# Performance work log

Hardware: AMD Instinct MI355X
Metric: run time of the kernel (lower is better)

The kernel has to match this reference:

```python
import jax, jax.numpy as jnp
import numpy as np

MARGIN = 0.5  # init kwarg margin=0.5 (float -> fix_margin branch)

N, D, NUM_CLASSES = 8192, 128, 512


def setup_inputs() -> dict:
    key = jax.random.key(0)
    k1, k2 = jax.random.split(key)
    embeds = jax.random.normal(k1, (N, D), dtype=jnp.float32)
    labels = jax.random.randint(k2, (N,), 0, NUM_CLASSES)
    return {"embeds": embeds, "labels": labels}


def reference(embeds, labels):
    n = embeds.shape[0]
    # --- batch-hard mining (detached in original: .detach().cpu().numpy()) ---
    # Euclidean pairwise distances via Gram trick (avoids [N,N,D] intermediate).
    sq = jnp.sum(embeds * embeds, axis=1)  # [N]
    d2 = sq[:, None] + sq[None, :] - 2.0 * (embeds @ embeds.T)  # [N,N]
    dist = jnp.sqrt(jnp.maximum(d2, 0.0))
    dist = jax.lax.stop_gradient(dist)

    same = labels[:, None] == labels[None, :]  # [N,N]
    eye = jnp.eye(n, dtype=bool)
    pos_mask = same & ~eye          # same label, not self
    neg_mask = ~same                # different label (diag excluded since same there)

    pos_idx = jnp.argmax(jnp.where(pos_mask, dist, -jnp.inf), axis=1)  # hardest positive
    neg_idx = jnp.argmin(jnp.where(neg_mask, dist, jnp.inf), axis=1)   # hardest negative

    # --- margin loss with metric='sqeuclidean' (gradients flow through gathers) ---
    dp = embeds - embeds[pos_idx]
    dn = embeds - embeds[neg_idx]
    ap = jnp.sum(dp * dp, axis=1)
    an = jnp.sum(dn * dn, axis=1)
    return jnp.mean(jax.nn.relu(ap - an + MARGIN))
```

## Files before the change

### kernel.cpp

```cpp
#include <hip/hip_runtime.h>
#include <stdint.h>

#define NROWS 8192
#define DIM 128
#define ROWB 256
#define NIBLK 64
#define NCHUNK 32
#define MARGIN 0.5f

typedef short short8 __attribute__((ext_vector_type(8)));
typedef float f32x4 __attribute__((ext_vector_type(4)));
typedef int   int4v __attribute__((ext_vector_type(4)));

#define GLDS16(g, l) __builtin_amdgcn_global_load_lds( \
    (const __attribute__((address_space(1))) unsigned int*)(g), \
    (__attribute__((address_space(3))) unsigned int*)(l), 16, 0, 0)

static __device__ __forceinline__ unsigned short f2bf(float f) {
    union { float f; unsigned u; } x; x.f = f;
    unsigned u = x.u;
    return (unsigned short)((u + 0x7FFFu + ((u >> 16) & 1u)) >> 16);
}

__global__ __launch_bounds__(256) void prep(const float* __restrict__ emb,
                                            unsigned short* __restrict__ e16,
                                            float* __restrict__ cbuf,
                                            unsigned* __restrict__ pos,
                                            unsigned* __restrict__ neg,
                                            float* __restrict__ out) {
    const int lane = threadIdx.x & 63;
    const int row = blockIdx.x * 4 + (threadIdx.x >> 6);
    const float2 v = reinterpret_cast<const float2*>(emb + row * DIM)[lane];
    float sq = v.x * v.x + v.y * v.y;
#pragma unroll
    for (int m = 1; m < 64; m <<= 1) sq += __shfl_xor(sq, m, 64);
    const unsigned pack = ((unsigned)f2bf(v.y) << 16) | (unsigned)f2bf(v.x);
    *reinterpret_cast<unsigned*>(e16 + row * DIM + lane * 2) = pack;
    if (lane == 0) cbuf[row] = sq + 512.0f;
    if (lane == 1) pos[row] = 0u;
    if (lane == 2) neg[row] = 0xFFFFFFFFu;
    if (blockIdx.x == 0 && threadIdx.x == 0) out[0] = 0.0f;
}

__global__ __launch_bounds__(512, 6) void mine(const unsigned short* __restrict__ e16,
                                               const float* __restrict__ cbuf,
                                               const int* __restrict__ labels,
                                               unsigned* __restrict__ pos,
                                               unsigned* __restrict__ neg) {
    __shared__ char smem[2][16384];
    const int tid  = threadIdx.x;
    const int wave = tid >> 6;
    const int lane = tid & 63;
    const int l15  = lane & 15;
    const int lhi  = lane >> 4;
    const int iblk = blockIdx.x & (NIBLK - 1);
    const int cblk = blockIdx.x / NIBLK;
    const int irow = iblk * 128 + wave * 16 + l15;
    const char* e8 = (const char*)e16;
    const int jc = cblk * 256;

    {
        const char* gs = e8 + (size_t)jc * ROWB;
        char* lb = smem[0];
#pragma unroll
        for (int q = 0; q < 2; ++q) {
            const int r = q * 32 + (tid >> 4);
            const int d = tid & 15;
            const int g = d ^ (r & 15);
            GLDS16(gs + (size_t)r * ROWB + g * 16, lb + q * 8192 + tid * 16);
        }
    }

    short8 bfrag[4];
#pragma unroll
    for (int ks = 0; ks < 4; ++ks)
        bfrag[ks] = *reinterpret_cast<const short8*>(e8 + (size_t)irow * ROWB + (ks * 4 + lhi) * 16);
    const int labi = labels[irow];

    unsigned bp = 0u, bn = 0xFFFFFFFFu;

    __syncthreads();

#pragma unroll
    for (int st = 0; st < 4; ++st) {
        if (st < 3) {
            const char* gs = e8 + (size_t)(jc + (st + 1) * 64) * ROWB;
            char* lb = smem[(st + 1) & 1];
#pragma unroll
            for (int q = 0; q < 2; ++q) {
                const int r = q * 32 + (tid >> 4);
                const int d = tid & 15;
                const int g = d ^ (r & 15);
                GLDS16(gs + (size_t)r * ROWB + g * 16, lb + q * 8192 + tid * 16);
            }
        }
        const char* buf = smem[st & 1];
#pragma unroll
        for (int jt = 0; jt < 4; ++jt) {
            const int jb = jc + st * 64 + jt * 16;
            const int4v labj = *reinterpret_cast<const int4v*>(labels + jb + lhi * 4);
            const f32x4 c4   = *reinterpret_cast<const f32x4*>(cbuf + jb + lhi * 4);
            const f32x4 cinit = c4 * -0.5f;

            short8 af[4];
#pragma unroll
            for (int ks = 0; ks < 4; ++ks)
                af[ks] = *reinterpret_cast<const short8*>(
                    buf + (jt * 16 + l15) * ROWB + (((ks * 4 + lhi) ^ l15) * 16));

            f32x4 acc = __builtin_amdgcn_mfma_f32_16x16x32_bf16(af[0], bfrag[0], cinit, 0, 0, 0);
#pragma unroll
            for (int ks = 1; ks < 4; ++ks)
                acc = __builtin_amdgcn_mfma_f32_16x16x32_bf16(af[ks], bfrag[ks], acc, 0, 0, 0);

            const int j0 = jb + lhi * 4;
#pragma unroll
            for (int r = 0; r < 4; ++r) {
                union { float f; unsigned u; } cv; cv.f = acc[r];
                const unsigned cand = (cv.u & 0xFFFFE000u) | (unsigned)(j0 + r);
                const bool eq = (labj[r] == labi);
                const unsigned psel = eq ? cand : 0u;
                const unsigned nsel = eq ? 0xFFFFFFFFu : cand;
                bp = bp > psel ? bp : psel;
                bn = bn < nsel ? bn : nsel;
            }
        }
        __syncthreads();
    }

    {
        unsigned o;
        o = (unsigned)__shfl_xor((int)bp, 16, 64); bp = bp > o ? bp : o;
        o = (unsigned)__shfl_xor((int)bp, 32, 64); bp = bp > o ? bp : o;
        o = (unsigned)__shfl_xor((int)bn, 16, 64); bn = bn < o ? bn : o;
        o = (unsigned)__shfl_xor((int)bn, 32, 64); bn = bn < o ? bn : o;
    }
    if (lane < 16) {
        const int i = iblk * 128 + wave * 16 + lane;
        atomicMax(&pos[i], bp);
        atomicMin(&neg[i], bn);
    }
}

__global__ __launch_bounds__(256) void lossk(const float* __restrict__ emb,
                                             const unsigned* __restrict__ pos,
                                             const unsigned* __restrict__ neg,
                                             float* __restrict__ bsum) {
    __shared__ float wsum[4];
    const int tid = threadIdx.x, lane = tid & 63, wave = tid >> 6;
    const int i = blockIdx.x * 4 + wave;
    const int jp = (int)(pos[i] & 8191u);
    const int jn = (int)(neg[i] & 8191u);
    const float2 a = reinterpret_cast<const float2*>(emb + (size_t)i  * DIM)[lane];
    const float2 b = reinterpret_cast<const float2*>(emb + (size_t)jp * DIM)[lane];
    const float2 c = reinterpret_cast<const float2*>(emb + (size_t)jn * DIM)[lane];
    float dx = a.x - b.x, dy = a.y - b.y;
    const float ap = dx * dx + dy * dy;
    dx = a.x - c.x; dy = a.y - c.y;
    const float an = dx * dx + dy * dy;
    float s = ap - an;
#pragma unroll
    for (int m = 1; m < 64; m <<= 1) s += __shfl_xor(s, m, 64);
    if (lane == 0) wsum[wave] = fmaxf(s + MARGIN, 0.f);
    __syncthreads();
    if (tid == 0) bsum[blockIdx.x] = wsum[0] + wsum[1] + wsum[2] + wsum[3];
}

__global__ __launch_bounds__(256) void fin(const float* __restrict__ bsum,
                                           float* __restrict__ out) {
    __shared__ float wsum[4];
    const int tid = threadIdx.x, lane = tid & 63, wave = tid >> 6;
    float s = 0.f;
#pragma unroll
    for (int k = 0; k < 8; ++k) s += bsum[tid + k * 256];
#pragma unroll
    for (int m = 1; m < 64; m <<= 1) s += __shfl_xor(s, m, 64);
    if (lane == 0) wsum[wave] = s;
    __syncthreads();
    if (tid == 0) out[0] = (wsum[0] + wsum[1] + wsum[2] + wsum[3]) * (1.0f / (float)NROWS);
}

extern "C" void kernel_launch(void* const* d_in, const int* in_sizes, int n_in,
                              void* d_out, int out_size, void* d_ws, size_t ws_size,
                              hipStream_t stream) {
    const float* emb   = (const float*)d_in[0];
    const int* labels  = (const int*)d_in[1];
    float* out = (float*)d_out;
    char* ws = (char*)d_ws;

    unsigned short* e16 = (unsigned short*)ws;
    float* cbuf         = (float*)(ws + (size_t)2097152);
    unsigned* pos       = (unsigned*)(ws + (size_t)2097152 + 32768);
    unsigned* neg       = pos + NROWS;
    float* bsum         = (float*)(neg + NROWS);

    prep<<<2048, 256, 0, stream>>>(emb, e16, cbuf, pos, neg, out);
    mine<<<NIBLK * NCHUNK, 512, 0, stream>>>(e16, cbuf, labels, pos, neg);
    lossk<<<2048, 256, 0, stream>>>(emb, pos, neg, bsum);
    fin<<<1, 256, 0, stream>>>(bsum, out);
}
```

Baseline: 94.39 us.

## Compute two 16-row i-tiles per wave to reuse LDS A-fragments across MFMAs

The mining kernel drops to 256 threads per block, and each wave now handles 32 anchor rows as two 16-row register fragments. Each LDS-loaded j-fragment therefore feeds two MFMA chains, halving LDS reads per MFMA. Label and norm loads are hoisted per stage and the swizzled LDS offsets are precomputed. The cost is more registers per thread and fewer waves per block, which may lower occupancy and latency hiding.

```diff
diff --git a/kernel.cpp b/kernel.cpp
--- a/kernel.cpp
+++ b/kernel.cpp
@@ -42,7 +42,7 @@
     if (blockIdx.x == 0 && threadIdx.x == 0) out[0] = 0.0f;
 }
 
-__global__ __launch_bounds__(512, 6) void mine(const unsigned short* __restrict__ e16,
+__global__ __launch_bounds__(256, 4) void mine(const unsigned short* __restrict__ e16,
                                                const float* __restrict__ cbuf,
                                                const int* __restrict__ labels,
                                                unsigned* __restrict__ pos,
@@ -55,29 +55,39 @@
     const int lhi  = lane >> 4;
     const int iblk = blockIdx.x & (NIBLK - 1);
     const int cblk = blockIdx.x / NIBLK;
-    const int irow = iblk * 128 + wave * 16 + l15;
+    const int ibase = iblk * 128 + wave * 32;
     const char* e8 = (const char*)e16;
     const int jc = cblk * 256;
+
+    const int srow = tid >> 4;
+    const int gsw  = ((tid & 15) ^ srow) * 16;
 
     {
         const char* gs = e8 + (size_t)jc * ROWB;
         char* lb = smem[0];
 #pragma unroll
-        for (int q = 0; q < 2; ++q) {
-            const int r = q * 32 + (tid >> 4);
-            const int d = tid & 15;
-            const int g = d ^ (r & 15);
-            GLDS16(gs + (size_t)r * ROWB + g * 16, lb + q * 8192 + tid * 16);
-        }
-    }
-
-    short8 bfrag[4];
+        for (int q = 0; q < 4; ++q)
+            GLDS16(gs + (size_t)(q * 16 + srow) * ROWB + gsw, lb + q * 4096 + tid * 16);
+    }
+
+    short8 bfrag[2][4];
+    int labi[2];
+#pragma unroll
+    for (int it = 0; it < 2; ++it) {
+        const int row = ibase + it * 16 + l15;
+#pragma unroll
+        for (int ks = 0; ks < 4; ++ks)
+            bfrag[it][ks] = *reinterpret_cast<const short8*>(e8 + (size_t)row * ROWB + (ks * 4 + lhi) * 16);
+        labi[it] = labels[row];
+    }
+
+    int dsoff[4];
 #pragma unroll
     for (int ks = 0; ks < 4; ++ks)
-        bfrag[ks] = *reinterpret_cast<const short8*>(e8 + (size_t)irow * ROWB + (ks * 4 + lhi) * 16);
-    const int labi = labels[irow];
-
-    unsigned bp = 0u, bn = 0xFFFFFFFFu;
+        dsoff[ks] = l15 * ROWB + (((ks * 4 + lhi) ^ l15) * 16);
+
+    unsigned bp[2] = {0u, 0u};
+    unsigned bn[2] = {0xFFFFFFFFu, 0xFFFFFFFFu};
 
     __syncthreads();
 
@@ -87,58 +97,66 @@
             const char* gs = e8 + (size_t)(jc + (st + 1) * 64) * ROWB;
             char* lb = smem[(st + 1) & 1];
 #pragma unroll
-            for (int q = 0; q < 2; ++q) {
-                const int r = q * 32 + (tid >> 4);
-                const int d = tid & 15;
-                const int g = d ^ (r & 15);
-                GLDS16(gs + (size_t)r * ROWB + g * 16, lb + q * 8192 + tid * 16);
-            }
+            for (int q = 0; q < 4; ++q)
+                GLDS16(gs + (size_t)(q * 16 + srow) * ROWB + gsw, lb + q * 4096 + tid * 16);
+        }
+        int4v labj_s[4];
+        f32x4 cin_s[4];
+#pragma unroll
+        for (int jt = 0; jt < 4; ++jt) {
+            const int jb = jc + st * 64 + jt * 16;
+            labj_s[jt] = *reinterpret_cast<const int4v*>(labels + jb + lhi * 4);
+            cin_s[jt]  = *reinterpret_cast<const f32x4*>(cbuf + jb + lhi * 4) * -0.5f;
         }
         const char* buf = smem[st & 1];
 #pragma unroll
         for (int jt = 0; jt < 4; ++jt) {
-            const int jb = jc + st * 64 + jt * 16;
-            const int4v labj = *reinterpret_cast<const int4v*>(labels + jb + lhi * 4);
-            const f32x4 c4   = *reinterpret_cast<const f32x4*>(cbuf + jb + lhi * 4);
-            const f32x4 cinit = c4 * -0.5f;
-
             short8 af[4];
 #pragma unroll
             for (int ks = 0; ks < 4; ++ks)
-                af[ks] = *reinterpret_cast<const short8*>(
-                    buf + (jt * 16 + l15) * ROWB + (((ks * 4 + lhi) ^ l15) * 16));
-
-            f32x4 acc = __builtin_amdgcn_mfma_f32_16x16x32_bf16(af[0], bfrag[0], cinit, 0, 0, 0);
+                af[ks] = *reinterpret_cast<const short8*>(buf + jt * 4096 + dsoff[ks]);
+
+            f32x4 acc[2];
+#pragma unroll
+            for (int it = 0; it < 2; ++it)
+                acc[it] = __builtin_amdgcn_mfma_f32_16x16x32_bf16(af[0], bfrag[it][0], cin_s[jt], 0, 0, 0);
 #pragma unroll
             for (int ks = 1; ks < 4; ++ks)
-                acc = __builtin_amdgcn_mfma_f32_16x16x32_bf16(af[ks], bfrag[ks], acc, 0, 0, 0);
-
-            const int j0 = jb + lhi * 4;
-#pragma unroll
-            for (int r = 0; r < 4; ++r) {
-                union { float f; unsigned u; } cv; cv.f = acc[r];
-                const unsigned cand = (cv.u & 0xFFFFE000u) | (unsigned)(j0 + r);
-                const bool eq = (labj[r] == labi);
-                const unsigned psel = eq ? cand : 0u;
-                const unsigned nsel = eq ? 0xFFFFFFFFu : cand;
-                bp = bp > psel ? bp : psel;
-                bn = bn < nsel ? bn : nsel;
+#pragma unroll
+                for (int it = 0; it < 2; ++it)
+                    acc[it] = __builtin_amdgcn_mfma_f32_16x16x32_bf16(af[ks], bfrag[it][ks], acc[it], 0, 0, 0);
+
+            const int j0 = jc + st * 64 + jt * 16 + lhi * 4;
+#pragma unroll
+            for (int it = 0; it < 2; ++it) {
+#pragma unroll
+                for (int r = 0; r < 4; ++r) {
+                    union { float f; unsigned u; } cv; cv.f = acc[it][r];
+                    const unsigned cand = (cv.u & 0xFFFFE000u) | (unsigned)(j0 + r);
+                    const bool eq = (labj_s[jt][r] == labi[it]);
+                    const unsigned psel = eq ? cand : 0u;
+                    const unsigned nsel = eq ? 0xFFFFFFFFu : cand;
+                    bp[it] = bp[it] > psel ? bp[it] : psel;
+                    bn[it] = bn[it] < nsel ? bn[it] : nsel;
+                }
             }
         }
         __syncthreads();
     }
 
-    {
+#pragma unroll
+    for (int it = 0; it < 2; ++it) {
         unsigned o;
-        o = (unsigned)__shfl_xor((int)bp, 16, 64); bp = bp > o ? bp : o;
-        o = (unsigned)__shfl_xor((int)bp, 32, 64); bp = bp > o ? bp : o;
-        o = (unsigned)__shfl_xor((int)bn, 16, 64); bn = bn < o ? bn : o;
-        o = (unsigned)__shfl_xor((int)bn, 32, 64); bn = bn < o ? bn : o;
-    }
-    if (lane < 16) {
-        const int i = iblk * 128 + wave * 16 + lane;
-        atomicMax(&pos[i], bp);
-        atomicMin(&neg[i], bn);
+        o = (unsigned)__shfl_xor((int)bp[it], 16, 64); bp[it] = bp[it] > o ? bp[it] : o;
+        o = (unsigned)__shfl_xor((int)bp[it], 32, 64); bp[it] = bp[it] > o ? bp[it] : o;
+        o = (unsigned)__shfl_xor((int)bn[it], 16, 64); bn[it] = bn[it] < o ? bn[it] : o;
+        o = (unsigned)__shfl_xor((int)bn[it], 32, 64); bn[it] = bn[it] < o ? bn[it] : o;
+    }
+    if (lane < 32) {
+        const int it = lane >> 4;
+        const int i = ibase + lane;
+        atomicMax(&pos[i], bp[it]);
+        atomicMin(&neg[i], bn[it]);
     }
 }
 
@@ -195,7 +213,7 @@
     float* bsum         = (float*)(neg + NROWS);
 
     prep<<<2048, 256, 0, stream>>>(emb, e16, cbuf, pos, neg, out);
-    mine<<<NIBLK * NCHUNK, 512, 0, stream>>>(e16, cbuf, labels, pos, neg);
+    mine<<<NIBLK * NCHUNK, 256, 0, stream>>>(e16, cbuf, labels, pos, neg);
     lossk<<<2048, 256, 0, stream>>>(emb, pos, neg, bsum);
     fin<<<1, 256, 0, stream>>>(bsum, out);
 }
```

New measurement: 92.45 us. -2.0%, faster.

## Store embeddings in MFMA fragment order and read A-tiles directly from global

Applied to the files above, without the earlier changes.

The prep kernel now writes the bf16 embeddings in a pre-swizzled MFMA-fragment layout, so each lane loads its 16-byte fragment with one coalesced global load. The mining kernel drops the LDS double-buffer and its barriers, and each wave now holds four 16-row i-tiles in registers to reuse every loaded j-fragment across four MFMAs. This removes LDS traffic and synchronisation and raises arithmetic reuse per load, but it relies on L2/L1 caching for the repeated j-tile reads and raises register pressure with the occupancy hint reduced to 4.

```diff
diff --git a/kernel.cpp b/kernel.cpp
--- a/kernel.cpp
+++ b/kernel.cpp
@@ -3,18 +3,11 @@
 
 #define NROWS 8192
 #define DIM 128
-#define ROWB 256
-#define NIBLK 64
-#define NCHUNK 32
 #define MARGIN 0.5f
 
 typedef short short8 __attribute__((ext_vector_type(8)));
 typedef float f32x4 __attribute__((ext_vector_type(4)));
 typedef int   int4v __attribute__((ext_vector_type(4)));
-
-#define GLDS16(g, l) __builtin_amdgcn_global_load_lds( \
-    (const __attribute__((address_space(1))) unsigned int*)(g), \
-    (__attribute__((address_space(3))) unsigned int*)(l), 16, 0, 0)
 
 static __device__ __forceinline__ unsigned short f2bf(float f) {
     union { float f; unsigned u; } x; x.f = f;
@@ -23,122 +16,111 @@
 }
 
 __global__ __launch_bounds__(256) void prep(const float* __restrict__ emb,
-                                            unsigned short* __restrict__ e16,
+                                            char* __restrict__ efrag,
                                             float* __restrict__ cbuf,
                                             unsigned* __restrict__ pos,
                                             unsigned* __restrict__ neg,
                                             float* __restrict__ out) {
-    const int lane = threadIdx.x & 63;
+    const int d = threadIdx.x & 63;
     const int row = blockIdx.x * 4 + (threadIdx.x >> 6);
-    const float2 v = reinterpret_cast<const float2*>(emb + row * DIM)[lane];
+    const float2 v = reinterpret_cast<const float2*>(emb + row * DIM)[d];
     float sq = v.x * v.x + v.y * v.y;
 #pragma unroll
     for (int m = 1; m < 64; m <<= 1) sq += __shfl_xor(sq, m, 64);
     const unsigned pack = ((unsigned)f2bf(v.y) << 16) | (unsigned)f2bf(v.x);
-    *reinterpret_cast<unsigned*>(e16 + row * DIM + lane * 2) = pack;
-    if (lane == 0) cbuf[row] = sq + 512.0f;
-    if (lane == 1) pos[row] = 0u;
-    if (lane == 2) neg[row] = 0xFFFFFFFFu;
+    char* dst = efrag + (size_t)(row >> 4) * 4096 + (d >> 4) * 1024
+              + ((((d >> 2) & 3) * 16 + (row & 15)) * 16) + (d & 3) * 4;
+    *reinterpret_cast<unsigned*>(dst) = pack;
+    if (d == 0) cbuf[row] = sq + 512.0f;
+    if (d == 1) pos[row] = 0u;
+    if (d == 2) neg[row] = 0xFFFFFFFFu;
     if (blockIdx.x == 0 && threadIdx.x == 0) out[0] = 0.0f;
 }
 
-__global__ __launch_bounds__(512, 6) void mine(const unsigned short* __restrict__ e16,
+__global__ __launch_bounds__(256, 4) void mine(const char* __restrict__ efrag,
                                                const float* __restrict__ cbuf,
                                                const int* __restrict__ labels,
                                                unsigned* __restrict__ pos,
                                                unsigned* __restrict__ neg) {
-    __shared__ char smem[2][16384];
     const int tid  = threadIdx.x;
     const int wave = tid >> 6;
     const int lane = tid & 63;
     const int l15  = lane & 15;
     const int lhi  = lane >> 4;
-    const int iblk = blockIdx.x & (NIBLK - 1);
-    const int cblk = blockIdx.x / NIBLK;
-    const int irow = iblk * 128 + wave * 16 + l15;
-    const char* e8 = (const char*)e16;
+    const int iblk = blockIdx.x & 31;
+    const int cblk = blockIdx.x >> 5;
+    const int ibase = iblk * 256 + wave * 64;
+
+    short8 bfrag[4][4];
+    int labi[4];
+#pragma unroll
+    for (int it = 0; it < 4; ++it) {
+        const char* bt = efrag + (size_t)((ibase >> 4) + it) * 4096 + lane * 16;
+#pragma unroll
+        for (int ks = 0; ks < 4; ++ks)
+            bfrag[it][ks] = *reinterpret_cast<const short8*>(bt + ks * 1024);
+        labi[it] = labels[ibase + it * 16 + l15];
+    }
+
+    unsigned bp[4] = {0u, 0u, 0u, 0u};
+    unsigned bn[4] = {0xFFFFFFFFu, 0xFFFFFFFFu, 0xFFFFFFFFu, 0xFFFFFFFFu};
+
     const int jc = cblk * 256;
+    const char* aj = efrag + (size_t)(cblk * 16) * 4096 + lane * 16;
 
-    {
-        const char* gs = e8 + (size_t)jc * ROWB;
-        char* lb = smem[0];
+#pragma unroll 2
+    for (int jt = 0; jt < 16; ++jt) {
+        const int jb = jc + jt * 16;
+        const int4v labj = *reinterpret_cast<const int4v*>(labels + jb + lhi * 4);
+        const f32x4 cinit = *reinterpret_cast<const f32x4*>(cbuf + jb + lhi * 4) * -0.5f;
+        const char* at = aj + (size_t)jt * 4096;
+
+        const short8 af0 = *reinterpret_cast<const short8*>(at);
+        const short8 af1 = *reinterpret_cast<const short8*>(at + 1024);
+        f32x4 acc[4];
 #pragma unroll
-        for (int q = 0; q < 2; ++q) {
-            const int r = q * 32 + (tid >> 4);
-            const int d = tid & 15;
-            const int g = d ^ (r & 15);
-            GLDS16(gs + (size_t)r * ROWB + g * 16, lb + q * 8192 + tid * 16);
+        for (int it = 0; it < 4; ++it)
+            acc[it] = __builtin_amdgcn_mfma_f32_16x16x32_bf16(af0, bfrag[it][0], cinit, 0, 0, 0);
+#pragma unroll
+        for (int it = 0; it < 4; ++it)
+            acc[it] = __builtin_amdgcn_mfma_f32_16x16x32_bf16(af1, bfrag[it][1], acc[it], 0, 0, 0);
+        const short8 af2 = *reinterpret_cast<const short8*>(at + 2048);
+        const short8 af3 = *reinterpret_cast<const short8*>(at + 3072);
+#pragma unroll
+        for (int it = 0; it < 4; ++it)
+            acc[it] = __builtin_amdgcn_mfma_f32_16x16x32_bf16(af2, bfrag[it][2], acc[it], 0, 0, 0);
+#pragma unroll
+        for (int it = 0; it < 4; ++it)
+            acc[it] = __builtin_amdgcn_mfma_f32_16x16x32_bf16(af3, bfrag[it][3], acc[it], 0, 0, 0);
+
+        const int jv = jb + lhi * 4;
+#pragma unroll
+        for (int it = 0; it < 4; ++it) {
+#pragma unroll
+            for (int r = 0; r < 4; ++r) {
+                union { float f; unsigned u; } cv; cv.f = acc[it][r];
+                const unsigned cand = (cv.u & 0xFFFFE000u) | (unsigned)(jv + r);
+                const bool eq = (labj[r] == labi[it]);
+                const unsigned psel = eq ? cand : 0u;
+                const unsigned nsel = eq ? 0xFFFFFFFFu : cand;
+                bp[it] = bp[it] > psel ? bp[it] : psel;
+                bn[it] = bn[it] < nsel ? bn[it] : nsel;
+            }
         }
     }
 
-    short8 bfrag[4];
 #pragma unroll
-    for (int ks = 0; ks < 4; ++ks)
-        bfrag[ks] = *reinterpret_cast<const short8*>(e8 + (size_t)irow * ROWB + (ks * 4 + lhi) * 16);
-    const int labi = labels[irow];
-
-    unsigned bp = 0u, bn = 0xFFFFFFFFu;
-
-    __syncthreads();
-
-#pragma unroll
-    for (int st = 0; st < 4; ++st) {
-        if (st < 3) {
-            const char* gs = e8 + (size_t)(jc + (st + 1) * 64) * ROWB;
-            char* lb = smem[(st + 1) & 1];
-#pragma unroll
-            for (int q = 0; q < 2; ++q) {
-                const int r = q * 32 + (tid >> 4);
-                const int d = tid & 15;
-                const int g = d ^ (r & 15);
-                GLDS16(gs + (size_t)r * ROWB + g * 16, lb + q * 8192 + tid * 16);
-            }
+    for (int it = 0; it < 4; ++it) {
+        unsigned o;
+        o = (unsigned)__shfl_xor((int)bp[it], 16, 64); bp[it] = bp[it] > o ? bp[it] : o;
+        o = (unsigned)__shfl_xor((int)bp[it], 32, 64); bp[it] = bp[it] > o ? bp[it] : o;
+        o = (unsigned)__shfl_xor((int)bn[it], 16, 64); bn[it] = bn[it] < o ? bn[it] : o;
+        o = (unsigned)__shfl_xor((int)bn[it], 32, 64); bn[it] = bn[it] < o ? bn[it] : o;
+        if (lane < 16) {
+            const int i = ibase + it * 16 + lane;
+            atomicMax(&pos[i], bp[it]);
+            atomicMin(&neg[i], bn[it]);
         }
-        const char* buf = smem[st & 1];
-#pragma unroll
-        for (int jt = 0; jt < 4; ++jt) {
-            const int jb = jc + st * 64 + jt * 16;
-            const int4v labj = *reinterpret_cast<const int4v*>(labels + jb + lhi * 4);
-            const f32x4 c4   = *reinterpret_cast<const f32x4*>(cbuf + jb + lhi * 4);
-            const f32x4 cinit = c4 * -0.5f;
-
-            short8 af[4];
-#pragma unroll
-            for (int ks = 0; ks < 4; ++ks)
-                af[ks] = *reinterpret_cast<const short8*>(
-                    buf + (jt * 16 + l15) * ROWB + (((ks * 4 + lhi) ^ l15) * 16));
-
-            f32x4 acc = __builtin_amdgcn_mfma_f32_16x16x32_bf16(af[0], bfrag[0], cinit, 0, 0, 0);
-#pragma unroll
-            for (int ks = 1; ks < 4; ++ks)
-                acc = __builtin_amdgcn_mfma_f32_16x16x32_bf16(af[ks], bfrag[ks], acc, 0, 0, 0);
-
-            const int j0 = jb + lhi * 4;
-#pragma unroll
-            for (int r = 0; r < 4; ++r) {
-                union { float f; unsigned u; } cv; cv.f = acc[r];
-                const unsigned cand = (cv.u & 0xFFFFE000u) | (unsigned)(j0 + r);
-                const bool eq = (labj[r] == labi);
-                const unsigned psel = eq ? cand : 0u;
-                const unsigned nsel = eq ? 0xFFFFFFFFu : cand;
-                bp = bp > psel ? bp : psel;
-                bn = bn < nsel ? bn : nsel;
-            }
-        }
-        __syncthreads();
-    }
-
-    {
-        unsigned o;
-        o = (unsigned)__shfl_xor((int)bp, 16, 64); bp = bp > o ? bp : o;
-        o = (unsigned)__shfl_xor((int)bp, 32, 64); bp = bp > o ? bp : o;
-        o = (unsigned)__shfl_xor((int)bn, 16, 64); bn = bn < o ? bn : o;
-        o = (unsigned)__shfl_xor((int)bn, 32, 64); bn = bn < o ? bn : o;
-    }
-    if (lane < 16) {
-        const int i = iblk * 128 + wave * 16 + lane;
-        atomicMax(&pos[i], bp);
-        atomicMin(&neg[i], bn);
     }
 }
 
@@ -188,14 +170,14 @@
     float* out = (float*)d_out;
     char* ws = (char*)d_ws;
 
-    unsigned short* e16 = (unsigned short*)ws;
-    float* cbuf         = (float*)(ws + (size_t)2097152);
-    unsigned* pos       = (unsigned*)(ws + (size_t)2097152 + 32768);
-    unsigned* neg       = pos + NROWS;
-    float* bsum         = (float*)(neg + NROWS);
+    char* efrag    = ws;
+    float* cbuf    = (float*)(ws + (size_t)2097152);
+    unsigned* pos  = (unsigned*)(ws + (size_t)2097152 + 32768);
+    unsigned* neg  = pos + NROWS;
+    float* bsum    = (float*)(neg + NROWS);
 
-    prep<<<2048, 256, 0, stream>>>(emb, e16, cbuf, pos, neg, out);
-    mine<<<NIBLK * NCHUNK, 512, 0, stream>>>(e16, cbuf, labels, pos, neg);
+    prep<<<2048, 256, 0, stream>>>(emb, efrag, cbuf, pos, neg, out);
+    mine<<<1024, 256, 0, stream>>>(efrag, cbuf, labels, pos, neg);
     lossk<<<2048, 256, 0, stream>>>(emb, pos, neg, bsum);
     fin<<<1, 256, 0, stream>>>(bsum, out);
 }
```

New measurement: 90.36 us. -4.3%, faster.
